# Kernel optimization log

Measured on AMD Instinct MI355X. Metric: run time of the kernel, lower is better.

## Reference

```python
import jax, jax.numpy as jnp
import numpy as np

B, L = 8, 512
EMB, NHEAD, HD = 512, 8, 64
FFN, NL = 2048, 6
VOCAB, NRE, RING_START, PAD, MAXLEN = 45, 20, 24, 0, 512
NOUT0 = VOCAB - NRE  # 25
NEG = -jnp.inf


def _ln(x, g, b, eps=1e-5):
    m = jnp.mean(x, -1, keepdims=True)
    v = jnp.mean((x - m) ** 2, -1, keepdims=True)
    return (x - m) * jax.lax.rsqrt(v + eps) * g + b


def setup_inputs():
    key = jax.random.key(0)
    ks = jax.random.split(key, 24)
    p = lambda k, shape: jax.random.normal(k, shape, jnp.float32) * 0.02
    return {
        "sequences": jax.random.randint(ks[0], (B, L), 1, VOCAB),  # avoid PAD=0
        "count_sequences": jax.random.randint(ks[1], (B, L), 0, MAXLEN),
        "graph_mask_sequences": jax.random.bernoulli(ks[2], 0.05, (B, L, VOCAB)),
        "valence_mask_sequences": jax.random.bernoulli(ks[3], 0.05, (B, L, VOCAB)),
        "linear_loc_squares": jax.random.randint(ks[4], (B, L, L), 0, MAXLEN + 1),
        "up_loc_squares": jax.random.randint(ks[5], (B, L, L), 0, MAXLEN + 1),
        "down_loc_squares": jax.random.randint(ks[6], (B, L, L), 0, MAXLEN + 1),
        "tok_emb": p(ks[7], (VOCAB, EMB)),
        "cnt_emb": p(ks[8], (MAXLEN, EMB)),
        "lin_loc_emb": p(ks[9], (MAXLEN + 1, NHEAD)),
        "up_loc_emb": p(ks[10], (MAXLEN + 1, NHEAD)),
        "down_loc_emb": p(ks[11], (MAXLEN + 1, NHEAD)),
        "in_proj_w": p(ks[12], (NL, 3 * EMB, EMB)),
        "in_proj_b": jnp.zeros((NL, 3 * EMB), jnp.float32),
        "out_w": p(ks[13], (NL, EMB, EMB)),
        "out_b": jnp.zeros((NL, EMB), jnp.float32),
        "ln1_g": jnp.ones((NL, EMB), jnp.float32),
        "ln1_b": jnp.zeros((NL, EMB), jnp.float32),
        "ln2_g": jnp.ones((NL, EMB), jnp.float32),
        "ln2_b": jnp.zeros((NL, EMB), jnp.float32),
        "ffn_w1": p(ks[14], (NL, FFN, EMB)),
        "ffn_b1": jnp.zeros((NL, FFN), jnp.float32),
        "ffn_w2": p(ks[15], (NL, EMB, FFN)),
        "ffn_b2": jnp.zeros((NL, EMB), jnp.float32),
        "fin_g": jnp.ones((EMB,), jnp.float32),
        "fin_b": jnp.zeros((EMB,), jnp.float32),
        "gen_w": p(ks[16], (NOUT0, EMB)),
        "gen_b": jnp.zeros((NOUT0,), jnp.float32),
        "ring_w0": p(ks[17], (EMB, EMB)),
        "ring_b0": jnp.zeros((EMB,), jnp.float32),
        "ring_w1": p(ks[18], (EMB, EMB)),
        "ring_b1": jnp.zeros((EMB,), jnp.float32),
    }


def _forward(tok_emb, cnt_emb, lin_loc_emb, up_loc_emb, down_loc_emb,
             in_proj_w, in_proj_b, out_w, out_b, ln1_g, ln1_b, ln2_g, ln2_b,
             ffn_w1, ffn_b1, ffn_w2, ffn_b2, fin_g, fin_b, gen_w, gen_b,
             ring_w0, ring_b0, ring_w1, ring_b1,
             sequences, count_sequences, graph_mask_sequences,
             valence_mask_sequences, linear_loc_squares, up_loc_squares,
             down_loc_squares):
    scale_e = jnp.sqrt(jnp.float32(EMB))
    x = tok_emb[sequences] * scale_e + cnt_emb[count_sequences] * scale_e  # (B,L,E)

    # per-head additive attention bias from three (B,L,L) index lookups
    bias = lin_loc_emb[linear_loc_squares] + up_loc_emb[up_loc_squares] + down_loc_emb[down_loc_squares]  # (B,L,L,H)
    bias = jnp.transpose(bias, (0, 3, 1, 2))  # (B,H,Lq,Lk)
    causal = jnp.tril(jnp.ones((L, L), bool))
    attn_bias = jnp.where(causal[None, None], bias, NEG)
    pad = sequences == PAD  # key padding
    attn_bias = jnp.where(pad[:, None, None, :], NEG, attn_bias)

    inv_sqrt_hd = 1.0 / jnp.sqrt(jnp.float32(HD))
    for i in range(NL):  # post-norm TransformerEncoderLayer, gelu
        qkv = jnp.einsum('ble,fe->blf', x, in_proj_w[i]) + in_proj_b[i]
        q, k, v = jnp.split(qkv, 3, axis=-1)
        q = q.reshape(B, L, NHEAD, HD)
        k = k.reshape(B, L, NHEAD, HD)
        v = v.reshape(B, L, NHEAD, HD)
        scores = jnp.einsum('bqhd,bkhd->bhqk', q, k) * inv_sqrt_hd + attn_bias
        a = jax.nn.softmax(scores, axis=-1)
        ctx = jnp.einsum('bhqk,bkhd->bqhd', a, v).reshape(B, L, EMB)
        attn_out = jnp.einsum('ble,fe->blf', ctx, out_w[i]) + out_b[i]
        x = _ln(x + attn_out, ln1_g[i], ln1_b[i])
        h = jax.nn.gelu(jnp.einsum('ble,fe->blf', x, ffn_w1[i]) + ffn_b1[i], approximate=False)
        ff = jnp.einsum('blf,ef->ble', h, ffn_w2[i]) + ffn_b2[i]
        x = _ln(x + ff, ln2_g[i], ln2_b[i])
    x = _ln(x, fin_g, fin_b)

    logits0 = jnp.einsum('ble,oe->blo', x, gen_w) + gen_b  # (B,L,NOUT0)

    # EdgeLogitLayer: scatter ring-start projections into NRE slots
    out0 = jnp.einsum('ble,he->blh', x, ring_w0) + ring_b0
    out1_ = jnp.einsum('ble,he->blh', x, ring_w1) + ring_b1
    ring_start = sequences == RING_START
    idx = jnp.where(ring_start, jnp.cumsum(ring_start.astype(jnp.int32), axis=1), 0)  # (B,L)
    bidx = jnp.arange(B)[:, None]
    slots = jnp.zeros((B, NRE + 1, EMB), x.dtype).at[bidx, idx].set(out1_, mode='drop')
    ring_tab = slots[:, 1:]  # drop slot 0 (non-ring-start writes)
    logits1 = jnp.einsum('ble,bre->blr', out0, ring_tab) * (EMB ** -0.5)

    logits = jnp.concatenate([logits0, logits1], axis=2)  # (B,L,VOCAB)
    logits = jnp.where(graph_mask_sequences, NEG, logits)
    logits = jnp.where(valence_mask_sequences, NEG, logits)
    return logits


def reference(sequences, count_sequences, graph_mask_sequences, valence_mask_sequences,
              linear_loc_squares, up_loc_squares, down_loc_squares,
              tok_emb, cnt_emb, lin_loc_emb, up_loc_emb, down_loc_emb,
              in_proj_w, in_proj_b, out_w, out_b, ln1_g, ln1_b, ln2_g, ln2_b,
              ffn_w1, ffn_b1, ffn_w2, ffn_b2, fin_g, fin_b, gen_w, gen_b,
              ring_w0, ring_b0, ring_w1, ring_b1):
    return _forward(tok_emb, cnt_emb, lin_loc_emb, up_loc_emb, down_loc_emb,
                    in_proj_w, in_proj_b, out_w, out_b, ln1_g, ln1_b, ln2_g, ln2_b,
                    ffn_w1, ffn_b1, ffn_w2, ffn_b2, fin_g, fin_b, gen_w, gen_b,
                    ring_w0, ring_b0, ring_w1, ring_b1,
                    sequences, count_sequences, graph_mask_sequences,
                    valence_mask_sequences, linear_loc_squares, up_loc_squares,
                    down_loc_squares)
```

## Files before the change

### kernel.cpp

```cpp
#include <hip/hip_runtime.h>
#include <cmath>

#define BB 8
#define LL 512
#define EMB 512
#define NHEAD 8
#define HD 64
#define FFN 2048
#define NL 6
#define VOCAB 45
#define NRE 20
#define RING_START 24
#define NOUT0 25
#define BL 4096

#define BIG_NEG -1.0e30f

typedef __bf16 bf16x8 __attribute__((ext_vector_type(8)));
typedef __bf16 bf16x4 __attribute__((ext_vector_type(4)));
typedef float f32x4 __attribute__((ext_vector_type(4)));

__device__ __forceinline__ void ld_g2l(const __bf16* g, __bf16* l) {
  __builtin_amdgcn_global_load_lds(
      (const __attribute__((address_space(1))) unsigned int*)g,
      (__attribute__((address_space(3))) unsigned int*)l, 16, 0, 0);
}

__global__ __launch_bounds__(256) void megacast_kernel(
    const float* __restrict__ s0, const float* __restrict__ s1,
    const float* __restrict__ s2, const float* __restrict__ s3,
    const float* __restrict__ s4, const float* __restrict__ s5,
    const float* __restrict__ s6, const float* __restrict__ s7,
    const float* __restrict__ s8, __bf16* __restrict__ dw,
    __bf16* __restrict__ dt) {
  const int gid = blockIdx.x * 256 + threadIdx.x;
  const int szs[9] = {589824, 196608, 786432, 786432, 32768,
                      32768,  513,    513,    513};
  const float* srcs[9] = {s0, s1, s2, s3, s4, s5, s6, s7, s8};
  int seg = 0, base = 0;
  while (seg < 9 && gid >= base + szs[seg]) { base += szs[seg]; seg++; }
  if (seg >= 9) return;
  const int local = gid - base;
  const float* src = srcs[seg];
  const float4 a = ((const float4*)src)[local * 2];
  const float4 b = ((const float4*)src)[local * 2 + 1];
  bf16x8 v;
  v[0] = (__bf16)a.x; v[1] = (__bf16)a.y; v[2] = (__bf16)a.z; v[3] = (__bf16)a.w;
  v[4] = (__bf16)b.x; v[5] = (__bf16)b.y; v[6] = (__bf16)b.z; v[7] = (__bf16)b.w;
  __bf16* dst = (seg < 6) ? (dw + (size_t)base * 8 + (size_t)local * 8)
                          : (dt + (size_t)(seg - 6) * 4104 + (size_t)local * 8);
  *(bf16x8*)dst = v;
}

__global__ __launch_bounds__(128) void embed_kernel(
    const int* __restrict__ seq, const int* __restrict__ cnt,
    const float* __restrict__ tok_emb, const float* __restrict__ cnt_emb,
    float* __restrict__ x, __bf16* __restrict__ xb) {
  const int row = blockIdx.x;
  const int t = seq[row];
  const int c = cnt[row];
  const float scale = 22.627416997969522f;
  const int j = threadIdx.x * 4;
  float4 tv = *(const float4*)(tok_emb + (size_t)t * EMB + j);
  float4 cv = *(const float4*)(cnt_emb + (size_t)c * EMB + j);
  float4 o;
  o.x = (tv.x + cv.x) * scale;
  o.y = (tv.y + cv.y) * scale;
  o.z = (tv.z + cv.z) * scale;
  o.w = (tv.w + cv.w) * scale;
  *(float4*)(x + (size_t)row * EMB + j) = o;
  bf16x4 h;
  h[0] = (__bf16)o.x; h[1] = (__bf16)o.y; h[2] = (__bf16)o.z; h[3] = (__bf16)o.w;
  *(bf16x4*)(xb + (size_t)row * EMB + j) = h;
}

__global__ __launch_bounds__(256) void bias_kernel(
    const int* __restrict__ lin_sq, const int* __restrict__ up_sq,
    const int* __restrict__ down_sq,
    const __bf16* __restrict__ tl16, const __bf16* __restrict__ tu16,
    const __bf16* __restrict__ td16,
    const int* __restrict__ seq, __bf16* __restrict__ bias) {
  __shared__ __bf16 Tl[513 * 8], Tu[513 * 8], Td[513 * 8];
  __shared__ int seqs[LL];
  const int tid = threadIdx.x;
  const int b = blockIdx.x >> 6;
  const int q0 = (blockIdx.x & 63) * 8;
  for (int i = tid; i < 513; i += 256) {
    *(bf16x8*)&Tl[i * 8] = *(const bf16x8*)&tl16[i * 8];
    *(bf16x8*)&Tu[i * 8] = *(const bf16x8*)&tu16[i * 8];
    *(bf16x8*)&Td[i * 8] = *(const bf16x8*)&td16[i * 8];
  }
  for (int i = tid; i < LL; i += 256) seqs[i] = seq[b * LL + i];
  __syncthreads();
  for (int q = q0; q < q0 + 8; q++) {
    const size_t rbase = ((size_t)(b * LL + q)) * LL;
    for (int k = tid; k <= q; k += 256) {
      const int li = lin_sq[rbase + k], ui = up_sq[rbase + k],
                di = down_sq[rbase + k];
      const bool valid = (seqs[k] != 0);
      bf16x8 a = *(const bf16x8*)&Tl[li * 8];
      bf16x8 u = *(const bf16x8*)&Tu[ui * 8];
      bf16x8 d = *(const bf16x8*)&Td[di * 8];
#pragma unroll
      for (int h = 0; h < NHEAD; h++) {
        float v = valid ? ((float)a[h] + (float)u[h] + (float)d[h])
                        : -INFINITY;
        bias[(((size_t)(b * NHEAD + h) * LL) + q) * LL + k] = (__bf16)v;
      }
    }
  }
}

template <int BM, int BN, int ACT, int OUTBF, int RES, int B2>
__global__ __launch_bounds__(256) void gemm_mfma_kernel(
    const __bf16* __restrict__ A, const __bf16* __restrict__ W,
    const float* __restrict__ bias, const float* __restrict__ bias2,
    float* __restrict__ C, __bf16* __restrict__ Cb,
    const float* __restrict__ Res, int N, int K, int lda) {
  constexpr int MI = BM / 32;
  constexpr int NI = BN / 32;
  constexpr int LV = (BM == 128 ? 4 : 2) + (BN == 128 ? 4 : 2);
  __shared__ __bf16 As[2][BM * 64];
  __shared__ __bf16 Ws[2][BN * 64];
  const int tid = threadIdx.x;
  const int lane = tid & 63, wave = tid >> 6;
  const int wm = wave >> 1, wn = wave & 1;
  const int q = lane >> 4, l15 = lane & 15;
  const int m0 = blockIdx.y * BM, n0 = blockIdx.x * BN;

  const int sr = tid >> 3;
  const int sc = (tid & 7) ^ (sr & 7);
  const __bf16* Ag = A + (size_t)(m0 + sr) * lda + sc * 8;
  const __bf16* Wg = W + (size_t)(n0 + sr) * lda + sc * 8;

  auto stage = [&](int buf, int k0) {
    __bf16* Al = &As[buf][tid * 8];
    __bf16* Wl = &Ws[buf][tid * 8];
    ld_g2l(Ag + k0, Al);
    ld_g2l(Ag + k0 + (size_t)32 * lda, Al + 2048);
    if constexpr (BM == 128) {
      ld_g2l(Ag + k0 + (size_t)64 * lda, Al + 4096);
      ld_g2l(Ag + k0 + (size_t)96 * lda, Al + 6144);
    }
    ld_g2l(Wg + k0, Wl);
    ld_g2l(Wg + k0 + (size_t)32 * lda, Wl + 2048);
    if constexpr (BN == 128) {
      ld_g2l(Wg + k0 + (size_t)64 * lda, Wl + 4096);
      ld_g2l(Wg + k0 + (size_t)96 * lda, Wl + 6144);
    }
  };

  f32x4 acc[MI][NI] = {};

  stage(0, 0);
  int cur = 0;
  for (int k0 = 0; k0 < K; k0 += 64) {
    if (k0 + 64 < K) {
      stage(cur ^ 1, k0 + 64);
      if constexpr (LV == 4)
        asm volatile("s_waitcnt vmcnt(4)" ::: "memory");
      else if constexpr (LV == 6)
        asm volatile("s_waitcnt vmcnt(6)" ::: "memory");
      else
        asm volatile("s_waitcnt vmcnt(8)" ::: "memory");
    } else {
      asm volatile("s_waitcnt vmcnt(0)" ::: "memory");
    }
    __builtin_amdgcn_s_barrier();
    __builtin_amdgcn_sched_barrier(0);
#pragma unroll
    for (int kh = 0; kh < 2; kh++) {
      bf16x8 af[MI], bfr[NI];
      const int ch = ((kh * 4 + q) ^ (l15 & 7)) * 8;
#pragma unroll
      for (int mi = 0; mi < MI; mi++)
        af[mi] = *(const bf16x8*)&As[cur]
                     [(wm * (BM / 2) + mi * 16 + l15) * 64 + ch];
#pragma unroll
      for (int ni = 0; ni < NI; ni++)
        bfr[ni] = *(const bf16x8*)&Ws[cur]
                      [(wn * (BN / 2) + ni * 16 + l15) * 64 + ch];
#pragma unroll
      for (int mi = 0; mi < MI; mi++)
#pragma unroll
        for (int ni = 0; ni < NI; ni++)
          acc[mi][ni] = __builtin_amdgcn_mfma_f32_16x16x32_bf16(
              af[mi], bfr[ni], acc[mi][ni], 0, 0, 0);
    }
    __builtin_amdgcn_sched_barrier(0);
    __builtin_amdgcn_s_barrier();
    cur ^= 1;
  }

#pragma unroll
  for (int ni = 0; ni < NI; ni++) {
    const int n = n0 + wn * (BN / 2) + ni * 16 + l15;
    const float bv = (B2 && n >= EMB) ? bias2[n - EMB] : bias[n];
#pragma unroll
    for (int mi = 0; mi < MI; mi++) {
#pragma unroll
      for (int r = 0; r < 4; r++) {
        const int m = m0 + wm * (BM / 2) + mi * 16 + q * 4 + r;
        float v = acc[mi][ni][r] + bv;
        if (RES) v += Res[(size_t)m * N + n];
        if (ACT == 1) v = 0.5f * v * (1.0f + erff(v * 0.70710678118654752f));
        if (OUTBF)
          Cb[(size_t)m * N + n] = (__bf16)v;
        else
          C[(size_t)m * N + n] = v;
      }
    }
  }
}

__global__ __launch_bounds__(256) void attn_tile2_kernel(
    const __bf16* __restrict__ qkv, const __bf16* __restrict__ bias,
    __bf16* __restrict__ Po, float2* __restrict__ Pml,
    __bf16* __restrict__ ctx) {
  __shared__ __bf16 Ks[64][72];
  __shared__ __bf16 Vt[64][72];
  __shared__ __bf16 Ps[64][72];
  const int tid = threadIdx.x;
  const int lane = tid & 63, w = tid >> 6;
  const int q = lane >> 4, l15 = lane & 15;
  const int bh = blockIdx.y;
  const int b = bh >> 3, h = bh & 7;
  const int pidx = blockIdx.x;
  int qt = 0, acc0 = 0;
  while (acc0 + (qt / 2 + 1) <= pidx) { acc0 += qt / 2 + 1; qt++; }
  const int j = pidx - acc0;
  const int q0 = qt * 64;
  const int slot = (bh * 8 + qt) * 4 + j;
  const bool direct = (qt <= 1);
  const float inv_sqrt_hd = 0.125f;

  const int srow = tid >> 2, c0 = (tid & 3) * 16;
  {
    const __bf16* qsrc =
        qkv + (size_t)(b * LL + q0 + srow) * 1536 + h * HD + c0;
    *(bf16x8*)&Ps[srow][c0] = *(const bf16x8*)qsrc;
    *(bf16x8*)&Ps[srow][c0 + 8] = *(const bf16x8*)(qsrc + 8);
  }
  __syncthreads();
  const bf16x8 aq0 = *(const bf16x8*)&Ps[w * 16 + l15][q * 8];
  const bf16x8 aq1 = *(const bf16x8*)&Ps[w * 16 + l15][32 + q * 8];

  f32x4 o4[4] = {};
  float m[4], l[4];
#pragma unroll
  for (int r = 0; r < 4; r++) { m[r] = -INFINITY; l[r] = 0.f; }

  const int ktEnd = (2 * j + 1 <= qt) ? (2 * j + 1) : qt;
  for (int kt = 2 * j; kt <= ktEnd; kt++) {
    const int k0 = kt * 64;
    __syncthreads();
    {
      const __bf16* src = qkv + (size_t)(b * LL + k0 + srow) * 1536 + h * HD;
      bf16x8 kv0 = *(const bf16x8*)(src + 512 + c0);
      bf16x8 kv1 = *(const bf16x8*)(src + 512 + c0 + 8);
      bf16x8 vv0 = *(const bf16x8*)(src + 1024 + c0);
      bf16x8 vv1 = *(const bf16x8*)(src + 1024 + c0 + 8);
      *(bf16x8*)&Ks[srow][c0] = kv0;
      *(bf16x8*)&Ks[srow][c0 + 8] = kv1;
#pragma unroll
      for (int jj = 0; jj < 8; jj++) {
        Vt[c0 + jj][srow] = vv0[jj];
        Vt[c0 + 8 + jj][srow] = vv1[jj];
      }
    }
    __syncthreads();

    f32x4 s4[4] = {};
#pragma unroll
    for (int ni = 0; ni < 4; ni++) {
      bf16x8 bk0 = *(const bf16x8*)&Ks[ni * 16 + l15][q * 8];
      bf16x8 bk1 = *(const bf16x8*)&Ks[ni * 16 + l15][32 + q * 8];
      s4[ni] =
          __builtin_amdgcn_mfma_f32_16x16x32_bf16(aq0, bk0, s4[ni], 0, 0, 0);
      s4[ni] =
          __builtin_amdgcn_mfma_f32_16x16x32_bf16(aq1, bk1, s4[ni], 0, 0, 0);
    }

    const bool diag = (kt == qt);
    const size_t bbase = ((size_t)bh * LL + (q0 + w * 16 + q * 4)) * LL + k0;
#pragma unroll
    for (int r = 0; r < 4; r++) {
      const int qrow = w * 16 + q * 4 + r;
      float sv[4];
#pragma unroll
      for (int ni = 0; ni < 4; ni++) {
        sv[ni] = s4[ni][r] * inv_sqrt_hd +
                 (float)bias[bbase + (size_t)r * LL + ni * 16 + l15];
        if (diag && (ni * 16 + l15 > qrow)) sv[ni] = -INFINITY;
      }
      float tm = fmaxf(fmaxf(sv[0], sv[1]), fmaxf(sv[2], sv[3]));
#pragma unroll
      for (int off = 1; off < 16; off <<= 1)
        tm = fmaxf(tm, __shfl_xor(tm, off, 16));
      const float mnew = fmaxf(m[r], tm);
      const float alpha = expf(m[r] - mnew);
      float rs = 0.f;
#pragma unroll
      for (int ni = 0; ni < 4; ni++) {
        const float p = expf(sv[ni] - mnew);
        Ps[qrow][ni * 16 + l15] = (__bf16)p;
        rs += p;
      }
#pragma unroll
      for (int off = 1; off < 16; off <<= 1) rs += __shfl_xor(rs, off, 16);
      l[r] = l[r] * alpha + rs;
      m[r] = mnew;
#pragma unroll
      for (int ni = 0; ni < 4; ni++) o4[ni][r] *= alpha;
    }
    __syncthreads();

    {
      bf16x8 ap0 = *(const bf16x8*)&Ps[w * 16 + l15][q * 8];
      bf16x8 ap1 = *(const bf16x8*)&Ps[w * 16 + l15][32 + q * 8];
#pragma unroll
      for (int ni = 0; ni < 4; ni++) {
        bf16x8 bv0 = *(const bf16x8*)&Vt[ni * 16 + l15][q * 8];
        bf16x8 bv1 = *(const bf16x8*)&Vt[ni * 16 + l15][32 + q * 8];
        o4[ni] =
            __builtin_amdgcn_mfma_f32_16x16x32_bf16(ap0, bv0, o4[ni], 0, 0, 0);
        o4[ni] =
            __builtin_amdgcn_mfma_f32_16x16x32_bf16(ap1, bv1, o4[ni], 0, 0, 0);
      }
    }
  }

  if (direct) {
#pragma unroll
    for (int r = 0; r < 4; r++) {
      const int qrow = w * 16 + q * 4 + r;
      const float inv = 1.0f / l[r];
      __bf16* dst = ctx + (size_t)(b * LL + q0 + qrow) * EMB + h * HD + l15;
#pragma unroll
      for (int ni = 0; ni < 4; ni++) dst[ni * 16] = (__bf16)(o4[ni][r] * inv);
    }
  } else {
#pragma unroll
    for (int r = 0; r < 4; r++) {
      const int qrow = w * 16 + q * 4 + r;
      if (l15 == 0)
        Pml[(size_t)slot * 64 + qrow] = make_float2(m[r], l[r]);
      __bf16* dst = Po + (size_t)slot * 4096 + qrow * 64 + l15;
#pragma unroll
      for (int ni = 0; ni < 4; ni++) dst[ni * 16] = (__bf16)o4[ni][r];
    }
  }
}

__global__ __launch_bounds__(256) void attn_combine_kernel(
    const __bf16* __restrict__ Po, const float2* __restrict__ Pml,
    __bf16* __restrict__ ctx) {
  const int tid = threadIdx.x;
  const int bh = blockIdx.x / 6;
  const int qt = (blockIdx.x % 6) + 2;
  const int b = bh >> 3, h = bh & 7;
  const int nsl = qt / 2 + 1;
  const int slot0 = (bh * 8 + qt) * 4;
  __shared__ float wls[4][64];
  __shared__ float invl[64];
  if (tid < 64) {
    float mg = -3.0e38f;
    for (int s = 0; s < nsl; s++)
      mg = fmaxf(mg, Pml[(size_t)(slot0 + s) * 64 + tid].x);
    float lsum = 0.f;
    for (int s = 0; s < nsl; s++) {
      const float2 ml = Pml[(size_t)(slot0 + s) * 64 + tid];
      const float wk = expf(ml.x - mg);
      wls[s][tid] = wk;
      lsum += ml.y * wk;
    }
    invl[tid] = 1.0f / lsum;
  }
  __syncthreads();
  const int row = tid >> 2, d0 = (tid & 3) * 16;
  float acc[16] = {};
  for (int s = 0; s < nsl; s++) {
    const __bf16* src = Po + (size_t)(slot0 + s) * 4096 + row * 64 + d0;
    const float wk = wls[s][row];
    bf16x8 v0 = *(const bf16x8*)src;
    bf16x8 v1 = *(const bf16x8*)(src + 8);
#pragma unroll
    for (int jj = 0; jj < 8; jj++) {
      acc[jj] += (float)v0[jj] * wk;
      acc[8 + jj] += (float)v1[jj] * wk;
    }
  }
  const float il = invl[row];
  bf16x8 o0, o1;
#pragma unroll
  for (int jj = 0; jj < 8; jj++) {
    o0[jj] = (__bf16)(acc[jj] * il);
    o1[jj] = (__bf16)(acc[8 + jj] * il);
  }
  __bf16* dst = ctx + (size_t)(b * LL + qt * 64 + row) * EMB + h * HD + d0;
  *(bf16x8*)dst = o0;
  *(bf16x8*)(dst + 8) = o1;
}

template <int NSUM>
__global__ __launch_bounds__(256) void add_ln_kernel(
    const float* __restrict__ xin, const float* __restrict__ g,
    const float* __restrict__ bta, float* __restrict__ out,
    __bf16* __restrict__ outb) {
  const int row = blockIdx.x;
  const int tid = threadIdx.x;
  float v0 = 0.f, v1 = 0.f;
#pragma unroll
  for (int sId = 0; sId < NSUM; sId++) {
    const float* xr = xin + (size_t)sId * BL * EMB + (size_t)row * EMB;
    v0 += xr[tid * 2];
    v1 += xr[tid * 2 + 1];
  }
  float s = v0 + v1, ss = v0 * v0 + v1 * v1;
#pragma unroll
  for (int off = 1; off < 64; off <<= 1) {
    s += __shfl_xor(s, off, 64);
    ss += __shfl_xor(ss, off, 64);
  }
  __shared__ float sbuf[8];
  const int wave = tid >> 6, lane = tid & 63;
  if (lane == 0) { sbuf[wave] = s; sbuf[4 + wave] = ss; }
  __syncthreads();
  s = sbuf[0] + sbuf[1] + sbuf[2] + sbuf[3];
  ss = sbuf[4] + sbuf[5] + sbuf[6] + sbuf[7];
  const float mean = s * (1.0f / EMB);
  const float var = ss * (1.0f / EMB) - mean * mean;
  const float rstd = rsqrtf(var + 1e-5f);
  const float o0 = (v0 - mean) * rstd * g[tid * 2] + bta[tid * 2];
  const float o1 = (v1 - mean) * rstd * g[tid * 2 + 1] + bta[tid * 2 + 1];
  float* orow = out + (size_t)row * EMB;
  orow[tid * 2] = o0;
  orow[tid * 2 + 1] = o1;
  if (outb) {
    __bf16* brow = outb + (size_t)row * EMB;
    brow[tid * 2] = (__bf16)o0;
    brow[tid * 2 + 1] = (__bf16)o1;
  }
}

__global__ __launch_bounds__(512) void ring_scatter_kernel(
    const int* __restrict__ seq, const float* __restrict__ o01,
    float* __restrict__ ring_tab) {
  const int b = blockIdx.x;
  const int tid = threadIdx.x;
  float* rt = ring_tab + (size_t)b * NRE * EMB;
  __shared__ int pos[NRE];
  __shared__ int wcnt[8];
  __shared__ int total;
  const bool flag = (seq[b * LL + tid] == RING_START);
  const unsigned long long msk = __ballot(flag);
  const int wave = tid >> 6, lane = tid & 63;
  if (lane == 0) wcnt[wave] = __popcll(msk);
  for (int i = tid; i < NRE * EMB; i += 512) rt[i] = 0.f;
  __syncthreads();
  if (flag) {
    int base = 0;
    for (int w2 = 0; w2 < wave; w2++) base += wcnt[w2];
    const int ord = base + __popcll(msk & ((1ull << lane) - 1ull));
    if (ord < NRE) pos[ord] = tid;
  }
  if (tid == 0) {
    int t = 0;
    for (int w2 = 0; w2 < 8; w2++) t += wcnt[w2];
    total = (t < NRE) ? t : NRE;
  }
  __syncthreads();
  const int n = total;
  for (int r = 0; r < n; r++) {
    const float* src = o01 + (size_t)(b * LL + pos[r]) * 1024 + 512;
    rt[r * EMB + tid] = src[tid];
  }
}

__global__ __launch_bounds__(256) void head_kernel(
    const float* __restrict__ xf, const float* __restrict__ o01,
    const float* __restrict__ ring_tab, const float* __restrict__ gen_w,
    const float* __restrict__ gen_b, const int* __restrict__ gmask,
    const int* __restrict__ vmask, float* __restrict__ out) {
  const int row = blockIdx.x;
  const int b = row >> 9;
  const int tid = threadIdx.x;
  __shared__ float xr[EMB], o0s[EMB];
  {
    float2 a = ((const float2*)(xf + (size_t)row * EMB))[tid];
    ((float2*)xr)[tid] = a;
    float2 c = ((const float2*)(o01 + (size_t)row * 1024))[tid];
    ((float2*)o0s)[tid] = c;
  }
  __syncthreads();
  const int wave = tid >> 6, lane = tid & 63;
  for (int o = wave; o < VOCAB; o += 4) {
    const float* wrow;
    const float* src;
    float bv, scale;
    if (o < NOUT0) {
      wrow = gen_w + (size_t)o * EMB;
      bv = gen_b[o];
      src = xr;
      scale = 1.0f;
    } else {
      wrow = ring_tab + ((size_t)b * NRE + (o - NOUT0)) * EMB;
      bv = 0.0f;
      src = o0s;
      scale = 0.044194173824159216f;
    }
    float sum = 0.f;
#pragma unroll
    for (int j = 0; j < 8; j++) {
      const int d = lane + 64 * j;
      sum += src[d] * wrow[d];
    }
#pragma unroll
    for (int off = 1; off < 64; off <<= 1) sum += __shfl_xor(sum, off, 64);
    if (lane == 0) {
      float v = sum * scale + bv;
      const size_t oidx = (size_t)row * VOCAB + o;
      if (gmask[oidx] != 0 || vmask[oidx] != 0) v = BIG_NEG;
      out[oidx] = v;
    }
  }
}

extern "C" void kernel_launch(void* const* d_in, const int* in_sizes, int n_in,
                              void* d_out, int out_size, void* d_ws,
                              size_t ws_size, hipStream_t stream) {
  const int* seq = (const int*)d_in[0];
  const int* cnt = (const int*)d_in[1];
  const int* gmask = (const int*)d_in[2];
  const int* vmask = (const int*)d_in[3];
  const int* lin_sq = (const int*)d_in[4];
  const int* up_sq = (const int*)d_in[5];
  const int* down_sq = (const int*)d_in[6];
  const float* tok_emb = (const float*)d_in[7];
  const float* cnt_emb = (const float*)d_in[8];
  const float* lin_e = (const float*)d_in[9];
  const float* up_e = (const float*)d_in[10];
  const float* down_e = (const float*)d_in[11];
  const float* in_proj_w = (const float*)d_in[12];
  const float* in_proj_b = (const float*)d_in[13];
  const float* out_w = (const float*)d_in[14];
  const float* out_b = (const float*)d_in[15];
  const float* ln1_g = (const float*)d_in[16];
  const float* ln1_b = (const float*)d_in[17];
  const float* ln2_g = (const float*)d_in[18];
  const float* ln2_b = (const float*)d_in[19];
  const float* ffn_w1 = (const float*)d_in[20];
  const float* ffn_b1 = (const float*)d_in[21];
  const float* ffn_w2 = (const float*)d_in[22];
  const float* ffn_b2 = (const float*)d_in[23];
  const float* fin_g = (const float*)d_in[24];
  const float* fin_b = (const float*)d_in[25];
  const float* gen_w = (const float*)d_in[26];
  const float* gen_b = (const float*)d_in[27];
  const float* ring_w0 = (const float*)d_in[28];
  const float* ring_b0 = (const float*)d_in[29];
  const float* ring_w1 = (const float*)d_in[30];
  const float* ring_b1 = (const float*)d_in[31];

  char* p = (char*)d_ws;
  auto alloc_f = [&](size_t n) { float* r = (float*)p; p += n * 4; return r; };
  auto alloc_h = [&](size_t n) { __bf16* r = (__bf16*)p; p += n * 2; return r; };

  float* x = alloc_f((size_t)BL * EMB);
  float* pbuf = alloc_f((size_t)BL * EMB);
  float* xfb = alloc_f((size_t)BL * EMB);
  float* o01b = alloc_f((size_t)BL * 1024);
  float* ringb = alloc_f((size_t)BB * NRE * EMB);
  float2* attn_pml = (float2*)alloc_f((size_t)2048 * 64 * 2);
  __bf16* attn_po = alloc_h((size_t)2048 * 4096);
  __bf16* biasb = alloc_h((size_t)BB * NHEAD * LL * LL);
  __bf16* xb = alloc_h((size_t)BL * EMB);
  __bf16* qkvb16 = alloc_h((size_t)BL * 3 * EMB);
  __bf16* ctxb = alloc_h((size_t)BL * EMB);
  __bf16* hb = alloc_h((size_t)BL * FFN);
  __bf16* xfb16 = alloc_h((size_t)BL * EMB);
  __bf16* wqkv = alloc_h((size_t)NL * 3 * EMB * EMB);
  __bf16* wout = alloc_h((size_t)NL * EMB * EMB);
  __bf16* wf1 = alloc_h((size_t)NL * FFN * EMB);
  __bf16* wf2 = alloc_h((size_t)NL * EMB * FFN);
  __bf16* wr01 = alloc_h((size_t)2 * EMB * EMB);
  __bf16* tl16 = hb;
  __bf16* tu16 = hb + 4104;
  __bf16* td16 = hb + 8208;

  megacast_kernel<<<9478, 256, 0, stream>>>(
      in_proj_w, out_w, ffn_w1, ffn_w2, ring_w0, ring_w1, lin_e, up_e, down_e,
      wqkv, tl16);

  embed_kernel<<<BL, 128, 0, stream>>>(seq, cnt, tok_emb, cnt_emb, x, xb);
  bias_kernel<<<BB * 64, 256, 0, stream>>>(lin_sq, up_sq, down_sq, tl16, tu16,
                                           td16, seq, biasb);

  for (int i = 0; i < NL; i++) {
    gemm_mfma_kernel<128, 128, 0, 1, 0, 0><<<dim3(12, 32), 256, 0, stream>>>(
        xb, wqkv + (size_t)i * 3 * EMB * EMB, in_proj_b + (size_t)i * 3 * EMB,
        nullptr, nullptr, qkvb16, nullptr, 3 * EMB, EMB, EMB);
    attn_tile2_kernel<<<dim3(20, 64), 256, 0, stream>>>(qkvb16, biasb, attn_po,
                                                        attn_pml, ctxb);
    attn_combine_kernel<<<384, 256, 0, stream>>>(attn_po, attn_pml, ctxb);
    gemm_mfma_kernel<64, 64, 0, 0, 1, 0><<<dim3(8, 64), 256, 0, stream>>>(
        ctxb, wout + (size_t)i * EMB * EMB, out_b + (size_t)i * EMB, nullptr,
        pbuf, nullptr, x, EMB, EMB, EMB);
    add_ln_kernel<1><<<BL, 256, 0, stream>>>(
        pbuf, ln1_g + (size_t)i * EMB, ln1_b + (size_t)i * EMB, x, xb);
    gemm_mfma_kernel<128, 128, 1, 1, 0, 0><<<dim3(16, 32), 256, 0, stream>>>(
        xb, wf1 + (size_t)i * FFN * EMB, ffn_b1 + (size_t)i * FFN, nullptr,
        nullptr, hb, nullptr, FFN, EMB, EMB);
    gemm_mfma_kernel<64, 64, 0, 0, 1, 0><<<dim3(8, 64), 256, 0, stream>>>(
        hb, wf2 + (size_t)i * EMB * FFN, ffn_b2 + (size_t)i * EMB, nullptr,
        pbuf, nullptr, x, EMB, FFN, FFN);
    add_ln_kernel<1><<<BL, 256, 0, stream>>>(
        pbuf, ln2_g + (size_t)i * EMB, ln2_b + (size_t)i * EMB, x, xb);
  }

  add_ln_kernel<1><<<BL, 256, 0, stream>>>(x, fin_g, fin_b, xfb, xfb16);
  gemm_mfma_kernel<64, 128, 0, 0, 0, 1><<<dim3(8, 64), 256, 0, stream>>>(
      xfb16, wr01, ring_b0, ring_b1, o01b, nullptr, nullptr, 1024, EMB, EMB);
  ring_scatter_kernel<<<BB, 512, 0, stream>>>(seq, o01b, ringb);
  head_kernel<<<BL, 256, 0, stream>>>(xfb, o01b, ringb, gen_w, gen_b, gmask,
                                      vmask, (float*)d_out);
}
```

Measured before the change: 903.1 us.

## Add XCD-aware block swizzle and split-K for the FFN down-projection GEMM

Adds an XCD-aware remap of the linear block index so that neighbouring tiles land on the same XCD, which should improve L2 reuse. The remap is applied in the GEMM and attention kernels. The FFN2 GEMM (K=2048) is also split into two K halves written to separate partial buffers. add_ln_kernel<2> is expected to sum those partials, which doubles the number of workgroups for a GEMM that only had 512 tiles. The cost is an extra fp32 partial write and read, and a doubled pbuf allocation.

```diff
diff --git a/kernel.cpp b/kernel.cpp
--- a/kernel.cpp
+++ b/kernel.cpp
@@ -24,6 +24,13 @@
   __builtin_amdgcn_global_load_lds(
       (const __attribute__((address_space(1))) unsigned int*)g,
       (__attribute__((address_space(3))) unsigned int*)l, 16, 0, 0);
+}
+
+__device__ __forceinline__ int xcd_swizzle_lin() {
+  const int nwg = gridDim.x * gridDim.y * gridDim.z;
+  int lin = blockIdx.x + gridDim.x * (blockIdx.y + gridDim.y * blockIdx.z);
+  if ((nwg & 7) == 0) lin = (lin & 7) * (nwg >> 3) + (lin >> 3);
+  return lin;
 }
 
 __global__ __launch_bounds__(256) void megacast_kernel(
@@ -111,7 +118,7 @@
   }
 }
 
-template <int BM, int BN, int ACT, int OUTBF, int RES, int B2>
+template <int BM, int BN, int ACT, int OUTBF, int RES, int B2, int SPLITK>
 __global__ __launch_bounds__(256) void gemm_mfma_kernel(
     const __bf16* __restrict__ A, const __bf16* __restrict__ W,
     const float* __restrict__ bias, const float* __restrict__ bias2,
@@ -126,12 +133,17 @@
   const int lane = tid & 63, wave = tid >> 6;
   const int wm = wave >> 1, wn = wave & 1;
   const int q = lane >> 4, l15 = lane & 15;
-  const int m0 = blockIdx.y * BM, n0 = blockIdx.x * BN;
+
+  const int lin = xcd_swizzle_lin();
+  const int bx = lin % gridDim.x;
+  const int by = (lin / gridDim.x) % gridDim.y;
+  const int kz = SPLITK ? (lin / (gridDim.x * gridDim.y)) : 0;
+  const int m0 = by * BM, n0 = bx * BN;
 
   const int sr = tid >> 3;
   const int sc = (tid & 7) ^ (sr & 7);
-  const __bf16* Ag = A + (size_t)(m0 + sr) * lda + sc * 8;
-  const __bf16* Wg = W + (size_t)(n0 + sr) * lda + sc * 8;
+  const __bf16* Ag = A + (size_t)(m0 + sr) * lda + sc * 8 + (size_t)kz * K;
+  const __bf16* Wg = W + (size_t)(n0 + sr) * lda + sc * 8 + (size_t)kz * K;
 
   auto stage = [&](int buf, int k0) {
     __bf16* Al = &As[buf][tid * 8];
@@ -192,22 +204,25 @@
     cur ^= 1;
   }
 
+  float* Cz = SPLITK ? (C + (size_t)kz * ((size_t)BL * N)) : C;
 #pragma unroll
   for (int ni = 0; ni < NI; ni++) {
     const int n = n0 + wn * (BN / 2) + ni * 16 + l15;
-    const float bv = (B2 && n >= EMB) ? bias2[n - EMB] : bias[n];
+    float bv = 0.f;
+    if (!SPLITK || kz == 0)
+      bv = (B2 && n >= EMB) ? bias2[n - EMB] : bias[n];
 #pragma unroll
     for (int mi = 0; mi < MI; mi++) {
 #pragma unroll
       for (int r = 0; r < 4; r++) {
         const int m = m0 + wm * (BM / 2) + mi * 16 + q * 4 + r;
         float v = acc[mi][ni][r] + bv;
-        if (RES) v += Res[(size_t)m * N + n];
+        if (RES && (!SPLITK || kz == 0)) v += Res[(size_t)m * N + n];
         if (ACT == 1) v = 0.5f * v * (1.0f + erff(v * 0.70710678118654752f));
         if (OUTBF)
           Cb[(size_t)m * N + n] = (__bf16)v;
         else
-          C[(size_t)m * N + n] = v;
+          Cz[(size_t)m * N + n] = v;
       }
     }
   }
@@ -223,9 +238,10 @@
   const int tid = threadIdx.x;
   const int lane = tid & 63, w = tid >> 6;
   const int q = lane >> 4, l15 = lane & 15;
-  const int bh = blockIdx.y;
+  const int lin = xcd_swizzle_lin();
+  const int pidx = lin % gridDim.x;
+  const int bh = lin / gridDim.x;
   const int b = bh >> 3, h = bh & 7;
-  const int pidx = blockIdx.x;
   int qt = 0, acc0 = 0;
   while (acc0 + (qt / 2 + 1) <= pidx) { acc0 += qt / 2 + 1; qt++; }
   const int j = pidx - acc0;
@@ -567,7 +583,7 @@
   auto alloc_h = [&](size_t n) { __bf16* r = (__bf16*)p; p += n * 2; return r; };
 
   float* x = alloc_f((size_t)BL * EMB);
-  float* pbuf = alloc_f((size_t)BL * EMB);
+  float* pbuf = alloc_f((size_t)2 * BL * EMB);
   float* xfb = alloc_f((size_t)BL * EMB);
   float* o01b = alloc_f((size_t)BL * 1024);
   float* ringb = alloc_f((size_t)BB * NRE * EMB);
@@ -597,29 +613,32 @@
                                            td16, seq, biasb);
 
   for (int i = 0; i < NL; i++) {
-    gemm_mfma_kernel<128, 128, 0, 1, 0, 0><<<dim3(12, 32), 256, 0, stream>>>(
+    gemm_mfma_kernel<128, 128, 0, 1, 0, 0, 0>
+        <<<dim3(12, 32), 256, 0, stream>>>(
         xb, wqkv + (size_t)i * 3 * EMB * EMB, in_proj_b + (size_t)i * 3 * EMB,
         nullptr, nullptr, qkvb16, nullptr, 3 * EMB, EMB, EMB);
     attn_tile2_kernel<<<dim3(20, 64), 256, 0, stream>>>(qkvb16, biasb, attn_po,
                                                         attn_pml, ctxb);
     attn_combine_kernel<<<384, 256, 0, stream>>>(attn_po, attn_pml, ctxb);
-    gemm_mfma_kernel<64, 64, 0, 0, 1, 0><<<dim3(8, 64), 256, 0, stream>>>(
+    gemm_mfma_kernel<64, 64, 0, 0, 1, 0, 0><<<dim3(8, 64), 256, 0, stream>>>(
         ctxb, wout + (size_t)i * EMB * EMB, out_b + (size_t)i * EMB, nullptr,
         pbuf, nullptr, x, EMB, EMB, EMB);
     add_ln_kernel<1><<<BL, 256, 0, stream>>>(
         pbuf, ln1_g + (size_t)i * EMB, ln1_b + (size_t)i * EMB, x, xb);
-    gemm_mfma_kernel<128, 128, 1, 1, 0, 0><<<dim3(16, 32), 256, 0, stream>>>(
+    gemm_mfma_kernel<128, 128, 1, 1, 0, 0, 0>
+        <<<dim3(16, 32), 256, 0, stream>>>(
         xb, wf1 + (size_t)i * FFN * EMB, ffn_b1 + (size_t)i * FFN, nullptr,
         nullptr, hb, nullptr, FFN, EMB, EMB);
-    gemm_mfma_kernel<64, 64, 0, 0, 1, 0><<<dim3(8, 64), 256, 0, stream>>>(
+    gemm_mfma_kernel<64, 64, 0, 0, 1, 0, 1>
+        <<<dim3(8, 64, 2), 256, 0, stream>>>(
         hb, wf2 + (size_t)i * EMB * FFN, ffn_b2 + (size_t)i * EMB, nullptr,
-        pbuf, nullptr, x, EMB, FFN, FFN);
-    add_ln_kernel<1><<<BL, 256, 0, stream>>>(
+        pbuf, nullptr, x, EMB, FFN / 2, FFN);
+    add_ln_kernel<2><<<BL, 256, 0, stream>>>(
         pbuf, ln2_g + (size_t)i * EMB, ln2_b + (size_t)i * EMB, x, xb);
   }
 
   add_ln_kernel<1><<<BL, 256, 0, stream>>>(x, fin_g, fin_b, xfb, xfb16);
-  gemm_mfma_kernel<64, 128, 0, 0, 0, 1><<<dim3(8, 64), 256, 0, stream>>>(
+  gemm_mfma_kernel<64, 128, 0, 0, 0, 1, 0><<<dim3(8, 64), 256, 0, stream>>>(
       xfb16, wr01, ring_b0, ring_b1, o01b, nullptr, nullptr, 1024, EMB, EMB);
   ring_scatter_kernel<<<BB, 512, 0, stream>>>(seq, o01b, ringb);
   head_kernel<<<BL, 256, 0, stream>>>(xfb, o01b, ringb, gen_w, gen_b, gmask,
```

After: 887.0 us. Within noise of the previous version (-1.8%).
